# Kernel tuning notes

Hardware: AMD Instinct MI355X
Metric: run time of the kernel (lower is better)

Reference implementation:

```python
import jax, jax.numpy as jnp
import numpy as np

N = 20000       # nodes
E = 320000      # edges
D_IN = 128
H = 512
OUT = 7
EPS = 1e-5


def setup_inputs() -> dict:
    key = jax.random.key(0)
    ks = jax.random.split(key, 16)
    def lin(k, fan_in, fan_out):
        bound = 1.0 / np.sqrt(fan_in)
        kw, kb = jax.random.split(k)
        W = jax.random.uniform(kw, (fan_in, fan_out), jnp.float32, -bound, bound)
        b = jax.random.uniform(kb, (fan_out,), jnp.float32, -bound, bound)
        return W, b
    x = jax.random.normal(ks[0], (N, D_IN), jnp.float32)
    edge_index = jax.random.randint(ks[1], (2, E), 0, N, dtype=jnp.int64)
    W1, b1 = lin(ks[2], D_IN, H)
    W2, b2 = lin(ks[3], H, H)
    W3, b3 = lin(ks[4], H, H)
    W4, b4 = lin(ks[5], H, H)
    ln_gamma = jnp.ones((H,), jnp.float32)
    ln_beta = jnp.zeros((H,), jnp.float32)
    W_out, b_out = lin(ks[6], H, OUT)
    return {"x": x, "edge_index": edge_index,
            "W1": W1, "b1": b1, "W2": W2, "b2": b2,
            "W3": W3, "b3": b3, "W4": W4, "b4": b4,
            "ln_gamma": ln_gamma, "ln_beta": ln_beta,
            "W_out": W_out, "b_out": b_out}


def _gcn_layer(x, W, b, src, dst, dinv):
    # transform, then symmetric-normalized gather/scatter-add (PyG GCNConv)
    h = x @ W                                    # [N, H]
    norm = dinv[src] * dinv[dst]                 # [E+N]
    msg = h[src] * norm[:, None]                 # gather + scale
    agg = jax.ops.segment_sum(msg, dst, num_segments=N)
    return agg + b


def reference(x, edge_index, W1, b1, W2, b2, W3, b3, W4, b4,
              ln_gamma, ln_beta, W_out, b_out):
    loops = jnp.arange(N, dtype=edge_index.dtype)
    src = jnp.concatenate([edge_index[0], loops])  # A + I self loops
    dst = jnp.concatenate([edge_index[1], loops])
    deg = jax.ops.segment_sum(jnp.ones_like(src, dtype=x.dtype), dst,
                              num_segments=N)
    dinv = jnp.where(deg > 0, jax.lax.rsqrt(deg), 0.0)

    def ln(h):
        mu = h.mean(-1, keepdims=True)
        var = h.var(-1, keepdims=True)
        return (h - mu) * jax.lax.rsqrt(var + EPS) * ln_gamma + ln_beta

    for W, b in ((W1, b1), (W2, b2), (W3, b3), (W4, b4)):
        x = jax.nn.relu(ln(_gcn_layer(x, W, b, src, dst, dinv)))
    g = x.mean(axis=0)           # mean pool over nodes -> [H]
    # dropout is identity in eval mode
    return g @ W_out + b_out     # [OUT]
```

## Files before the change

kernel.cpp:

```cpp
#include <hip/hip_runtime.h>

#define HID 512
#define OUTD 7
#define EPSV 1e-5f
#define PB 256
#define PR 32

typedef __attribute__((ext_vector_type(8))) short bf16x8;
typedef __attribute__((ext_vector_type(4))) float f32x4;
typedef __attribute__((ext_vector_type(2))) float f32x2;
typedef unsigned short ushort_t;
typedef unsigned int uint_t;
typedef unsigned char uchar_t;

__device__ __forceinline__ ushort_t f2bf(float f) {
    uint_t u = __float_as_uint(f);
    u = (u + 0x7fffu + ((u >> 16) & 1u)) >> 16;
    return (ushort_t)u;
}
__device__ __forceinline__ float bflo(uint_t u) { return __uint_as_float(u << 16); }
__device__ __forceinline__ float bfhi(uint_t u) { return __uint_as_float(u & 0xffff0000u); }

__device__ __forceinline__ void acc16(const uint4& v, f32x2* a) {
    a[0] += __builtin_amdgcn_cvt_pk_f32_fp8(v.x, false);
    a[1] += __builtin_amdgcn_cvt_pk_f32_fp8(v.x, true);
    a[2] += __builtin_amdgcn_cvt_pk_f32_fp8(v.y, false);
    a[3] += __builtin_amdgcn_cvt_pk_f32_fp8(v.y, true);
    a[4] += __builtin_amdgcn_cvt_pk_f32_fp8(v.z, false);
    a[5] += __builtin_amdgcn_cvt_pk_f32_fp8(v.z, true);
    a[6] += __builtin_amdgcn_cvt_pk_f32_fp8(v.w, false);
    a[7] += __builtin_amdgcn_cvt_pk_f32_fp8(v.w, true);
}
__device__ __forceinline__ uint_t enc4(float a, float b, float c, float d) {
    uint_t r = __builtin_amdgcn_cvt_pk_fp8_f32(a, b, 0, false);
    r = __builtin_amdgcn_cvt_pk_fp8_f32(c, d, r, true);
    return r;
}

__device__ __forceinline__ void gload_lds16(const ushort_t* g, ushort_t* l) {
    __builtin_amdgcn_global_load_lds(
        (const __attribute__((address_space(1))) uint_t*)g,
        (__attribute__((address_space(3))) uint_t*)l, 16, 0, 0);
}

__global__ __launch_bounds__(256) void deg_wtrans(
        const int* __restrict__ dst, int* __restrict__ deg, int E, int degB,
        const float* __restrict__ W0, const float* __restrict__ W1,
        const float* __restrict__ W2, const float* __restrict__ W3,
        ushort_t* __restrict__ T0, ushort_t* __restrict__ T1,
        ushort_t* __restrict__ T2, ushort_t* __restrict__ T3) {
    __shared__ ushort_t tile[32][33];
    if ((int)blockIdx.x < degB) {
        int e = blockIdx.x * 256 + threadIdx.x;
        if (e < E) atomicAdd(&deg[dst[e]], 1);
        return;
    }
    int id = blockIdx.x - degB;
    const float* W; ushort_t* T; int K;
    if (id < 64)       { W = W0; T = T0; K = 128; }
    else if (id < 320) { W = W1; T = T1; K = 512; id -= 64; }
    else if (id < 576) { W = W2; T = T2; K = 512; id -= 320; }
    else               { W = W3; T = T3; K = 512; id -= 576; }
    const int tn = id & 15;
    const int tk = id >> 4;
    const int t = threadIdx.x;
    const int r = t >> 3;
    const int c4 = (t & 7) * 4;
    const float4 v = *(const float4*)&W[(size_t)(tk * 32 + r) * HID + tn * 32 + c4];
    tile[r][c4 + 0] = f2bf(v.x); tile[r][c4 + 1] = f2bf(v.y);
    tile[r][c4 + 2] = f2bf(v.z); tile[r][c4 + 3] = f2bf(v.w);
    __syncthreads();
    ushort4 ov = make_ushort4(tile[c4 + 0][r], tile[c4 + 1][r],
                              tile[c4 + 2][r], tile[c4 + 3][r]);
    *(ushort4*)&T[(size_t)(tn * 32 + r) * K + tk * 32 + c4] = ov;
}


__global__ void scan1(const int* __restrict__ deg, int* __restrict__ off,
                      int* __restrict__ partial, float* __restrict__ dinv, int N) {
    __shared__ int s[256];
    const int t = threadIdx.x;
    const int i = blockIdx.x * 256 + t;
    int d = (i < N) ? deg[i] : 0;
    if (i < N) dinv[i] = rsqrtf((float)(d + 1));
    s[t] = d;
    __syncthreads();
#pragma unroll
    for (int ofs = 1; ofs < 256; ofs <<= 1) {
        int v = (t >= ofs) ? s[t - ofs] : 0;
        __syncthreads();
        s[t] += v;
        __syncthreads();
    }
    if (i < N) off[i] = s[t] - d;
    if (t == 255) partial[blockIdx.x] = s[255];
}

__global__ void scan23(int* __restrict__ off, const int* __restrict__ partial,
                       int* __restrict__ cursor, int N, int E, int nb) {
    __shared__ int s[256];
    __shared__ int ex[256];
    const int t = threadIdx.x;
    int d = (t < nb) ? partial[t] : 0;
    s[t] = d;
    __syncthreads();
#pragma unroll
    for (int ofs = 1; ofs < 256; ofs <<= 1) {
        int v = (t >= ofs) ? s[t - ofs] : 0;
        __syncthreads();
        s[t] += v;
        __syncthreads();
    }
    ex[t] = s[t] - d;
    __syncthreads();
    int i = blockIdx.x * 256 + t;
    if (i < N) {
        int v = off[i] + ex[i >> 8];
        off[i] = v;
        cursor[i] = v;
    } else if (i == N) {
        off[N] = E;
    }
}


__global__ void fill_cvt(const int* __restrict__ src, const int* __restrict__ dst,
                         int* __restrict__ cursor, int* __restrict__ srcs, int E,
                         const float* __restrict__ x, const float* __restrict__ dinv,
                         ushort_t* __restrict__ xb, int pairs) {
    int i = blockIdx.x * blockDim.x + threadIdx.x;
    if (i < E) { int p = atomicAdd(&cursor[dst[i]], 1); srcs[p] = src[i]; return; }
    i -= E;
    if (i < pairs) {
        float dr = dinv[i >> 6];
        float a = x[2 * i] * dr, b = x[2 * i + 1] * dr;
        uint_t d = __builtin_amdgcn_cvt_pk_fp8_f32(a, b, 0, false);
        xb[i] = (ushort_t)(d & 0xffffu);
    }
}


__global__ __launch_bounds__(256) void csr_agg_512(
        const uchar_t* __restrict__ xs, const int* __restrict__ off,
        const int* __restrict__ srcs, const float* __restrict__ dinv,
        ushort_t* __restrict__ ax, int N) {
    int gtid = blockIdx.x * 256 + threadIdx.x;
    int r = gtid >> 6, lane = gtid & 63;
    if (r >= N) return;
    const int half = lane >> 5, l32 = lane & 31;
    const uint4* xb = (const uint4*)xs;
    f32x2 a[8];
#pragma unroll
    for (int q = 0; q < 8; q++) a[q] = (f32x2){0.f, 0.f};
    if (half == 0) {
        uint4 v = xb[(size_t)r * 32 + l32];
        acc16(v, a);
    }
    int e = off[r];
    const int e1 = off[r + 1];
    for (; e + 8 <= e1; e += 8) {
        int si[4]; uint4 vi[4];
#pragma unroll
        for (int j = 0; j < 4; j++) si[j] = srcs[e + 2 * j + half];
#pragma unroll
        for (int j = 0; j < 4; j++) vi[j] = xb[(size_t)si[j] * 32 + l32];
#pragma unroll
        for (int j = 0; j < 4; j++) acc16(vi[j], a);
    }
    for (; e < e1; e += 2) {
        int idx = e + half;
        bool valid = idx < e1;
        int s = srcs[valid ? idx : e];
        uint4 v = xb[(size_t)s * 32 + l32];
        if (!valid) { v.x = 0; v.y = 0; v.z = 0; v.w = 0; }
        acc16(v, a);
    }
#pragma unroll
    for (int q = 0; q < 8; q++) {
        a[q][0] += __shfl_xor(a[q][0], 32);
        a[q][1] += __shfl_xor(a[q][1], 32);
    }
    {
        float dr = dinv[r];
        const int b = half * 4;
        uint_t w0 = (uint_t)f2bf(a[b + 0][0] * dr) | ((uint_t)f2bf(a[b + 0][1] * dr) << 16);
        uint_t w1 = (uint_t)f2bf(a[b + 1][0] * dr) | ((uint_t)f2bf(a[b + 1][1] * dr) << 16);
        uint_t w2 = (uint_t)f2bf(a[b + 2][0] * dr) | ((uint_t)f2bf(a[b + 2][1] * dr) << 16);
        uint_t w3 = (uint_t)f2bf(a[b + 3][0] * dr) | ((uint_t)f2bf(a[b + 3][1] * dr) << 16);
        ((uint4*)ax)[(size_t)r * 64 + l32 * 2 + half] = make_uint4(w0, w1, w2, w3);
    }
}

__global__ __launch_bounds__(256) void csr_agg_128(
        const uchar_t* __restrict__ xs, const int* __restrict__ off,
        const int* __restrict__ srcs, const float* __restrict__ dinv,
        ushort_t* __restrict__ ax, int N) {
    int gtid = blockIdx.x * 256 + threadIdx.x;
    int r = gtid >> 6, lane = gtid & 63;
    if (r >= N) return;
    const int sub = lane >> 3, l8 = lane & 7;
    const uint4* xb = (const uint4*)xs;
    f32x2 a[8];
#pragma unroll
    for (int q = 0; q < 8; q++) a[q] = (f32x2){0.f, 0.f};
    if (sub == 0) {
        uint4 v = xb[(size_t)r * 8 + l8];
        acc16(v, a);
    }
    const int e1 = off[r + 1];
    for (int e = off[r]; e < e1; e += 8) {
        int idx = e + sub;
        bool valid = idx < e1;
        int s = srcs[valid ? idx : e];
        uint4 v = xb[(size_t)s * 8 + l8];
        if (!valid) { v.x = 0; v.y = 0; v.z = 0; v.w = 0; }
        acc16(v, a);
    }
#pragma unroll
    for (int q = 0; q < 8; q++) {
        a[q][0] += __shfl_xor(a[q][0], 8);  a[q][1] += __shfl_xor(a[q][1], 8);
        a[q][0] += __shfl_xor(a[q][0], 16); a[q][1] += __shfl_xor(a[q][1], 16);
        a[q][0] += __shfl_xor(a[q][0], 32); a[q][1] += __shfl_xor(a[q][1], 32);
    }
    if (sub < 2) {
        float dr = dinv[r];
        const int b = sub * 4;
        uint_t w0 = (uint_t)f2bf(a[b + 0][0] * dr) | ((uint_t)f2bf(a[b + 0][1] * dr) << 16);
        uint_t w1 = (uint_t)f2bf(a[b + 1][0] * dr) | ((uint_t)f2bf(a[b + 1][1] * dr) << 16);
        uint_t w2 = (uint_t)f2bf(a[b + 2][0] * dr) | ((uint_t)f2bf(a[b + 2][1] * dr) << 16);
        uint_t w3 = (uint_t)f2bf(a[b + 3][0] * dr) | ((uint_t)f2bf(a[b + 3][1] * dr) << 16);
        ((uint4*)ax)[(size_t)r * 16 + l8 * 2 + sub] = make_uint4(w0, w1, w2, w3);
    }
}


__global__ __launch_bounds__(256) void gemm_mfma(
        const ushort_t* __restrict__ A, const ushort_t* __restrict__ Wt,
        const float* __restrict__ bias, ushort_t* __restrict__ C, int M, int K, int MB) {
    __shared__ __align__(16) ushort_t AsL[128 * 64];
    __shared__ __align__(16) ushort_t BsL[128 * 64];
    const int id = blockIdx.x;
    const int mb = (id >> 5) * 8 + (id & 7);
    const int nbk = (id >> 3) & 3;
    if (mb >= MB) return;
    const int t = threadIdx.x;
    const int wave = t >> 6, lane = t & 63;
    const int m0 = mb * 128, n0 = nbk * 128;
    const int wm = (wave & 1) * 64, wn = (wave >> 1) * 64;
    const int quad = lane >> 4, l16 = lane & 15;
    const int srow = lane >> 3;
    const int schunk = (lane & 7) ^ srow;
    const int sw = (l16 & 7) << 4;

    f32x4 acc[4][4];
#pragma unroll
    for (int i = 0; i < 4; i++)
#pragma unroll
        for (int j = 0; j < 4; j++) acc[i][j] = (f32x4){0.f, 0.f, 0.f, 0.f};

    for (int k0 = 0; k0 < K; k0 += 64) {
#pragma unroll
        for (int j = 0; j < 4; j++) {
            const int c = wave * 4 + j;
            int gm = m0 + 8 * c + srow;
            if (gm >= M) gm = M - 1;
            gload_lds16(A + (size_t)gm * K + k0 + (schunk << 3), AsL + c * 512);
            gload_lds16(Wt + (size_t)(n0 + 8 * c + srow) * K + k0 + (schunk << 3),
                        BsL + c * 512);
        }
        __syncthreads();
#pragma unroll
        for (int kk = 0; kk < 2; kk++) {
            const int kb = (kk * 4 + quad) << 4;
            bf16x8 af[4], bfr[4];
#pragma unroll
            for (int jn = 0; jn < 4; jn++)
                bfr[jn] = *(const bf16x8*)((const char*)BsL
                              + (wn + jn * 16 + l16) * 128 + (kb ^ sw));
#pragma unroll
            for (int i = 0; i < 4; i++)
                af[i] = *(const bf16x8*)((const char*)AsL
                              + (wm + i * 16 + l16) * 128 + (kb ^ sw));
#pragma unroll
            for (int i = 0; i < 4; i++)
#pragma unroll
                for (int jn = 0; jn < 4; jn++)
                    acc[i][jn] = __builtin_amdgcn_mfma_f32_16x16x32_bf16(
                                     af[i], bfr[jn], acc[i][jn], 0, 0, 0);
        }
        __syncthreads();
    }
#pragma unroll
    for (int i = 0; i < 4; i++) {
#pragma unroll
        for (int jn = 0; jn < 4; jn++) {
            int gn = n0 + wn + jn * 16 + l16;
            float bv = bias[gn];
#pragma unroll
            for (int rg = 0; rg < 4; rg++) {
                int gm = m0 + wm + i * 16 + quad * 4 + rg;
                if (gm < M) C[(size_t)gm * HID + gn] = f2bf(acc[i][jn][rg] + bv);
            }
        }
    }
}


__global__ void ln_relu(const ushort_t* __restrict__ h, const float* __restrict__ gamma,
                        const float* __restrict__ beta, const float* __restrict__ dinv,
                        void* __restrict__ optr, int N) {
    int gtid = blockIdx.x * blockDim.x + threadIdx.x;
    int r = gtid >> 6, lane = gtid & 63;
    if (r >= N) return;
    uint4 v = ((const uint4*)(h + (size_t)r * HID))[lane];
    float f[8] = {bflo(v.x), bfhi(v.x), bflo(v.y), bfhi(v.y),
                  bflo(v.z), bfhi(v.z), bflo(v.w), bfhi(v.w)};
    float s = 0.f, q = 0.f;
#pragma unroll
    for (int j = 0; j < 8; j++) { s += f[j]; q += f[j] * f[j]; }
#pragma unroll
    for (int ofs = 32; ofs > 0; ofs >>= 1) {
        s += __shfl_xor(s, ofs);
        q += __shfl_xor(q, ofs);
    }
    float mu  = s * (1.0f / HID);
    float var = q * (1.0f / HID) - mu * mu;
    float rs  = rsqrtf(var + EPSV);
    float dr  = dinv[r];
    const float4* gp = (const float4*)gamma;
    const float4* bp = (const float4*)beta;
    float4 g0 = gp[2 * lane], g1 = gp[2 * lane + 1];
    float4 b0 = bp[2 * lane], b1 = bp[2 * lane + 1];
    float gg[8] = {g0.x, g0.y, g0.z, g0.w, g1.x, g1.y, g1.z, g1.w};
    float bb[8] = {b0.x, b0.y, b0.z, b0.w, b1.x, b1.y, b1.z, b1.w};
    float o[8];
#pragma unroll
    for (int j = 0; j < 8; j++)
        o[j] = fmaxf((f[j] - mu) * rs * gg[j] + bb[j], 0.f) * dr;
    uint2 ov;
    ov.x = enc4(o[0], o[1], o[2], o[3]);
    ov.y = enc4(o[4], o[5], o[6], o[7]);
    ((uint2*)optr)[(size_t)r * 64 + lane] = ov;
}


__global__ __launch_bounds__(256) void ln_pool(
        const ushort_t* __restrict__ h, const float* __restrict__ gamma,
        const float* __restrict__ beta, float* __restrict__ pbuf, int N) {
    __shared__ float sred[4][64][8];
    const int t = threadIdx.x;
    const int sub = t >> 6, lane = t & 63;
    const float4* gp = (const float4*)gamma;
    const float4* bp = (const float4*)beta;
    float4 g0 = gp[2 * lane], g1 = gp[2 * lane + 1];
    float4 b0 = bp[2 * lane], b1 = bp[2 * lane + 1];
    float gg[8] = {g0.x, g0.y, g0.z, g0.w, g1.x, g1.y, g1.z, g1.w};
    float bb[8] = {b0.x, b0.y, b0.z, b0.w, b1.x, b1.y, b1.z, b1.w};
    float colacc[8] = {0.f, 0.f, 0.f, 0.f, 0.f, 0.f, 0.f, 0.f};
    const int step = PB * 4;
    for (int r = blockIdx.x * 4 + sub; r < N; r += step) {
        uint4 v = ((const uint4*)(h + (size_t)r * HID))[lane];
        float f[8] = {bflo(v.x), bfhi(v.x), bflo(v.y), bfhi(v.y),
                      bflo(v.z), bfhi(v.z), bflo(v.w), bfhi(v.w)};
        float s = 0.f, q = 0.f;
#pragma unroll
        for (int j = 0; j < 8; j++) { s += f[j]; q += f[j] * f[j]; }
#pragma unroll
        for (int ofs = 32; ofs > 0; ofs >>= 1) {
            s += __shfl_xor(s, ofs);
            q += __shfl_xor(q, ofs);
        }
        float mu  = s * (1.0f / HID);
        float var = q * (1.0f / HID) - mu * mu;
        float rs  = rsqrtf(var + EPSV);
#pragma unroll
        for (int j = 0; j < 8; j++)
            colacc[j] += fmaxf((f[j] - mu) * rs * gg[j] + bb[j], 0.f);
    }
#pragma unroll
    for (int j = 0; j < 8; j++) sred[sub][lane][j] = colacc[j];
    __syncthreads();
    if (sub == 0) {
        float4 o0, o1;
        o0.x = sred[0][lane][0] + sred[1][lane][0] + sred[2][lane][0] + sred[3][lane][0];
        o0.y = sred[0][lane][1] + sred[1][lane][1] + sred[2][lane][1] + sred[3][lane][1];
        o0.z = sred[0][lane][2] + sred[1][lane][2] + sred[2][lane][2] + sred[3][lane][2];
        o0.w = sred[0][lane][3] + sred[1][lane][3] + sred[2][lane][3] + sred[3][lane][3];
        o1.x = sred[0][lane][4] + sred[1][lane][4] + sred[2][lane][4] + sred[3][lane][4];
        o1.y = sred[0][lane][5] + sred[1][lane][5] + sred[2][lane][5] + sred[3][lane][5];
        o1.z = sred[0][lane][6] + sred[1][lane][6] + sred[2][lane][6] + sred[3][lane][6];
        o1.w = sred[0][lane][7] + sred[1][lane][7] + sred[2][lane][7] + sred[3][lane][7];
        float* pb = pbuf + (size_t)blockIdx.x * HID + lane * 8;
        ((float4*)pb)[0] = o0;
        ((float4*)pb)[1] = o1;
    }
}


__global__ __launch_bounds__(256) void pool_reduce(
        const float* __restrict__ pbuf, float* __restrict__ pbuf2) {
    const int t = threadIdx.x;
    const int b = blockIdx.x;
    const int R = PB / PR;
    float2 s = make_float2(0.f, 0.f);
#pragma unroll
    for (int u = 0; u < R; u++) {
        const float2 v = ((const float2*)(pbuf + (size_t)(b * R + u) * HID))[t];
        s.x += v.x; s.y += v.y;
    }
    ((float2*)(pbuf2 + (size_t)b * HID))[t] = s;
}


__global__ void out_kernel(const float* __restrict__ pbuf2, const float* __restrict__ Wout,
                           const float* __restrict__ bout, float* __restrict__ out, int N) {
    __shared__ float red[256];
    int t = threadIdx.x;
    float g0 = 0.f, g1 = 0.f;
#pragma unroll
    for (int p = 0; p < PR; p += 8) {
#pragma unroll
        for (int u = 0; u < 8; u++) {
            const float2 v = ((const float2*)(pbuf2 + (size_t)(p + u) * HID))[t];
            g0 += v.x; g1 += v.y;
        }
    }
    float invn = 1.0f / (float)N;
    for (int o = 0; o < OUTD; o++) {
        float pr = g0 * Wout[(2 * t) * OUTD + o] + g1 * Wout[(2 * t + 1) * OUTD + o];
        red[t] = pr;
        __syncthreads();
        for (int sft = 128; sft > 0; sft >>= 1) {
            if (t < sft) red[t] += red[t + sft];
            __syncthreads();
        }
        if (t == 0) out[o] = red[0] * invn + bout[o];
        __syncthreads();
    }
}


extern "C" void kernel_launch(void* const* d_in, const int* in_sizes, int n_in,
                              void* d_out, int out_size, void* d_ws, size_t ws_size,
                              hipStream_t stream) {
    const float* x  = (const float*)d_in[0];
    const int*   ei = (const int*)d_in[1];
    const int N = in_sizes[0] / 128;
    const int E = in_sizes[1] / 2;
    const int* src = ei;
    const int* dst = ei + E;
    const float* Ws[4] = {(const float*)d_in[2], (const float*)d_in[4],
                          (const float*)d_in[6], (const float*)d_in[8]};
    const float* bs[4] = {(const float*)d_in[3], (const float*)d_in[5],
                          (const float*)d_in[7], (const float*)d_in[9]};
    const float* gamma = (const float*)d_in[10];
    const float* beta  = (const float*)d_in[11];
    const float* Wout  = (const float*)d_in[12];
    const float* bout  = (const float*)d_in[13];
    float* out = (float*)d_out;

    char* p = (char*)d_ws;
    ushort_t* axb = (ushort_t*)p;  p += sizeof(ushort_t) * (size_t)N * HID;
    ushort_t* hb  = (ushort_t*)p;  p += sizeof(ushort_t) * (size_t)N * HID;
    uchar_t*  ho8 = (uchar_t*)p;   p += (size_t)N * HID;
    uchar_t*  xb8 = ho8;
    ushort_t* Wt[4];
    Wt[0] = (ushort_t*)p;          p += sizeof(ushort_t) * 128 * HID;
    Wt[1] = (ushort_t*)p;          p += sizeof(ushort_t) * HID * HID;
    Wt[2] = (ushort_t*)p;          p += sizeof(ushort_t) * HID * HID;
    Wt[3] = (ushort_t*)p;          p += sizeof(ushort_t) * HID * HID;
    float* dinv  = (float*)p;      p += sizeof(float) * N;
    float* pbuf  = (float*)p;      p += sizeof(float) * PB * HID;
    float* pbuf2 = (float*)p;      p += sizeof(float) * PR * HID;
    int* deg    = (int*)p;         p += sizeof(int) * N;
    int* off    = (int*)p;         p += sizeof(int) * (N + 4);
    int* cursor = (int*)p;         p += sizeof(int) * N;
    int* partial= (int*)p;         p += sizeof(int) * 256;
    int* srcs   = (int*)p;

    const int nb = (N + 255) / 256;
    const int MB = (N + 127) / 128;
    const int gemm_blocks = 32 * ((MB + 7) / 8);
    const int degB = (E + 255) / 256;

    hipMemsetAsync(deg, 0, sizeof(int) * N, stream);
    deg_wtrans<<<degB + 832, 256, 0, stream>>>(dst, deg, E, degB,
                                               Ws[0], Ws[1], Ws[2], Ws[3],
                                               Wt[0], Wt[1], Wt[2], Wt[3]);
    scan1<<<nb, 256, 0, stream>>>(deg, off, partial, dinv, N);
    scan23<<<(N + 256) / 256, 256, 0, stream>>>(off, partial, cursor, N, E, nb);
    {
        int pairs = N * 64;
        int tot = E + pairs;
        fill_cvt<<<(tot + 255) / 256, 256, 0, stream>>>(src, dst, cursor, srcs, E,
                                                        x, dinv, (ushort_t*)xb8, pairs);
    }

    for (int l = 0; l < 4; l++) {
        const int K = (l == 0) ? 128 : HID;
        if (l == 0)
            csr_agg_128<<<(N * 64 + 255) / 256, 256, 0, stream>>>(xb8, off, srcs, dinv, axb, N);
        else
            csr_agg_512<<<(N * 64 + 255) / 256, 256, 0, stream>>>(ho8, off, srcs, dinv, axb, N);
        gemm_mfma<<<gemm_blocks, 256, 0, stream>>>(axb, Wt[l], bs[l], hb, N, K, MB);
        if (l < 3)
            ln_relu<<<(N * 64 + 255) / 256, 256, 0, stream>>>(hb, gamma, beta, dinv, ho8, N);
        else
            ln_pool<<<PB, 256, 0, stream>>>(hb, gamma, beta, pbuf, N);
    }
    pool_reduce<<<PR, 256, 0, stream>>>(pbuf, pbuf2);
    out_kernel<<<1, 256, 0, stream>>>(pbuf2, Wout, bout, out, N);
}
```

Baseline: 362.5 us.

## Bucket CSR neighbor lists by source range and fold pool reduction into output kernel

Edge counts are now kept per (destination, source-chunk) pair across 10 chunks, and the fill step places each edge into its chunk's slot. Each node's neighbor list therefore comes out roughly sorted by source index, which should improve cache locality for the feature gathers in the aggregation kernels. Separately, the pool_reduce kernel is removed and out_kernel sums all 256 partial rows itself, saving one launch but running that sum in a single block. In exchange, the degree and fill passes do twice the atomics and need ten times the count and cursor memory.

```diff
diff --git a/kernel.cpp b/kernel.cpp
--- a/kernel.cpp
+++ b/kernel.cpp
@@ -4,7 +4,7 @@
 #define OUTD 7
 #define EPSV 1e-5f
 #define PB 256
-#define PR 32
+#define NCH 10
 
 typedef __attribute__((ext_vector_type(8))) short bf16x8;
 typedef __attribute__((ext_vector_type(4))) float f32x4;
@@ -44,7 +44,8 @@
 }
 
 __global__ __launch_bounds__(256) void deg_wtrans(
-        const int* __restrict__ dst, int* __restrict__ deg, int E, int degB,
+        const int* __restrict__ src, const int* __restrict__ dst,
+        int* __restrict__ deg, int* __restrict__ deg10, int E, int degB, int sh,
         const float* __restrict__ W0, const float* __restrict__ W1,
         const float* __restrict__ W2, const float* __restrict__ W3,
         ushort_t* __restrict__ T0, ushort_t* __restrict__ T1,
@@ -52,7 +53,11 @@
     __shared__ ushort_t tile[32][33];
     if ((int)blockIdx.x < degB) {
         int e = blockIdx.x * 256 + threadIdx.x;
-        if (e < E) atomicAdd(&deg[dst[e]], 1);
+        if (e < E) {
+            int d = dst[e];
+            atomicAdd(&deg[d], 1);
+            atomicAdd(&deg10[d * NCH + (src[e] >> sh)], 1);
+        }
         return;
     }
     int id = blockIdx.x - degB;
@@ -97,7 +102,8 @@
 }
 
 __global__ void scan23(int* __restrict__ off, const int* __restrict__ partial,
-                       int* __restrict__ cursor, int N, int E, int nb) {
+                       const int* __restrict__ deg10, int* __restrict__ cursor10,
+                       int N, int E, int nb) {
     __shared__ int s[256];
     __shared__ int ex[256];
     const int t = threadIdx.x;
@@ -117,7 +123,12 @@
     if (i < N) {
         int v = off[i] + ex[i >> 8];
         off[i] = v;
-        cursor[i] = v;
+        int base = v;
+#pragma unroll
+        for (int c = 0; c < NCH; c++) {
+            cursor10[i * NCH + c] = base;
+            base += deg10[i * NCH + c];
+        }
     } else if (i == N) {
         off[N] = E;
     }
@@ -125,11 +136,16 @@
 
 
 __global__ void fill_cvt(const int* __restrict__ src, const int* __restrict__ dst,
-                         int* __restrict__ cursor, int* __restrict__ srcs, int E,
+                         int* __restrict__ cursor10, int* __restrict__ srcs, int E, int sh,
                          const float* __restrict__ x, const float* __restrict__ dinv,
                          ushort_t* __restrict__ xb, int pairs) {
     int i = blockIdx.x * blockDim.x + threadIdx.x;
-    if (i < E) { int p = atomicAdd(&cursor[dst[i]], 1); srcs[p] = src[i]; return; }
+    if (i < E) {
+        int sv = src[i];
+        int p = atomicAdd(&cursor10[dst[i] * NCH + (sv >> sh)], 1);
+        srcs[p] = sv;
+        return;
+    }
     i -= E;
     if (i < pairs) {
         float dr = dinv[i >> 6];
@@ -397,33 +413,15 @@
 }
 
 
-__global__ __launch_bounds__(256) void pool_reduce(
-        const float* __restrict__ pbuf, float* __restrict__ pbuf2) {
-    const int t = threadIdx.x;
-    const int b = blockIdx.x;
-    const int R = PB / PR;
-    float2 s = make_float2(0.f, 0.f);
-#pragma unroll
-    for (int u = 0; u < R; u++) {
-        const float2 v = ((const float2*)(pbuf + (size_t)(b * R + u) * HID))[t];
-        s.x += v.x; s.y += v.y;
-    }
-    ((float2*)(pbuf2 + (size_t)b * HID))[t] = s;
-}
-
-
-__global__ void out_kernel(const float* __restrict__ pbuf2, const float* __restrict__ Wout,
+__global__ void out_kernel(const float* __restrict__ pbuf, const float* __restrict__ Wout,
                            const float* __restrict__ bout, float* __restrict__ out, int N) {
     __shared__ float red[256];
     int t = threadIdx.x;
     float g0 = 0.f, g1 = 0.f;
-#pragma unroll
-    for (int p = 0; p < PR; p += 8) {
-#pragma unroll
-        for (int u = 0; u < 8; u++) {
-            const float2 v = ((const float2*)(pbuf2 + (size_t)(p + u) * HID))[t];
-            g0 += v.x; g1 += v.y;
-        }
+#pragma unroll 8
+    for (int p = 0; p < PB; p++) {
+        const float2 v = ((const float2*)(pbuf + (size_t)p * HID))[t];
+        g0 += v.x; g1 += v.y;
     }
     float invn = 1.0f / (float)N;
     for (int o = 0; o < OUTD; o++) {
@@ -459,6 +457,9 @@
     const float* bout  = (const float*)d_in[13];
     float* out = (float*)d_out;
 
+    int sh = 11;
+    while (((N - 1) >> sh) >= NCH) sh++;
+
     char* p = (char*)d_ws;
     ushort_t* axb = (ushort_t*)p;  p += sizeof(ushort_t) * (size_t)N * HID;
     ushort_t* hb  = (ushort_t*)p;  p += sizeof(ushort_t) * (size_t)N * HID;
@@ -471,28 +472,28 @@
     Wt[3] = (ushort_t*)p;          p += sizeof(ushort_t) * HID * HID;
     float* dinv  = (float*)p;      p += sizeof(float) * N;
     float* pbuf  = (float*)p;      p += sizeof(float) * PB * HID;
-    float* pbuf2 = (float*)p;      p += sizeof(float) * PR * HID;
-    int* deg    = (int*)p;         p += sizeof(int) * N;
-    int* off    = (int*)p;         p += sizeof(int) * (N + 4);
-    int* cursor = (int*)p;         p += sizeof(int) * N;
-    int* partial= (int*)p;         p += sizeof(int) * 256;
-    int* srcs   = (int*)p;
+    int* deg     = (int*)p;        p += sizeof(int) * N;
+    int* deg10   = (int*)p;        p += sizeof(int) * N * NCH;
+    int* cursor10= (int*)p;        p += sizeof(int) * N * NCH;
+    int* off     = (int*)p;        p += sizeof(int) * (N + 4);
+    int* partial = (int*)p;        p += sizeof(int) * 256;
+    int* srcs    = (int*)p;
 
     const int nb = (N + 255) / 256;
     const int MB = (N + 127) / 128;
     const int gemm_blocks = 32 * ((MB + 7) / 8);
     const int degB = (E + 255) / 256;
 
-    hipMemsetAsync(deg, 0, sizeof(int) * N, stream);
-    deg_wtrans<<<degB + 832, 256, 0, stream>>>(dst, deg, E, degB,
+    hipMemsetAsync(deg, 0, sizeof(int) * N * (1 + NCH), stream);
+    deg_wtrans<<<degB + 832, 256, 0, stream>>>(src, dst, deg, deg10, E, degB, sh,
                                                Ws[0], Ws[1], Ws[2], Ws[3],
                                                Wt[0], Wt[1], Wt[2], Wt[3]);
     scan1<<<nb, 256, 0, stream>>>(deg, off, partial, dinv, N);
-    scan23<<<(N + 256) / 256, 256, 0, stream>>>(off, partial, cursor, N, E, nb);
+    scan23<<<(N + 256) / 256, 256, 0, stream>>>(off, partial, deg10, cursor10, N, E, nb);
     {
         int pairs = N * 64;
         int tot = E + pairs;
-        fill_cvt<<<(tot + 255) / 256, 256, 0, stream>>>(src, dst, cursor, srcs, E,
+        fill_cvt<<<(tot + 255) / 256, 256, 0, stream>>>(src, dst, cursor10, srcs, E, sh,
                                                         x, dinv, (ushort_t*)xb8, pairs);
     }
 
@@ -508,6 +509,5 @@
         else
             ln_pool<<<PB, 256, 0, stream>>>(hb, gamma, beta, pbuf, N);
     }
-    pool_reduce<<<PR, 256, 0, stream>>>(pbuf, pbuf2);
-    out_kernel<<<1, 256, 0, stream>>>(pbuf2, Wout, bout, out, N);
-}
+    out_kernel<<<1, 256, 0, stream>>>(pbuf, Wout, bout, out, N);
+}
```

Result: slower. 380.7 us (+5.0%).

## Fuse LayerNorm+ReLU and pooling into GEMM via last-block-per-row-tile epilogue

Applied to the files above, without the earlier changes.

Each of the four column-tile GEMM blocks for a 128-row tile increments an atomic counter after writing its part. The last block to arrive re-reads the full 128x512 bf16 rows and applies LayerNorm+ReLU: it writes the fp8 scaled output, or in the final layer accumulates per-tile column sums for pooling. This removes the separate ln_relu, ln_pool and pool_reduce launches. The cost is that the LN work is serialized onto one block per row tile, and it adds atomics and threadfences. The out_kernel now sums the roughly 157 per-tile partial buffers serially.

```diff
diff --git a/kernel.cpp b/kernel.cpp
--- a/kernel.cpp
+++ b/kernel.cpp
@@ -3,8 +3,7 @@
 #define HID 512
 #define OUTD 7
 #define EPSV 1e-5f
-#define PB 256
-#define PR 32
+#define MBPAD 256
 
 typedef __attribute__((ext_vector_type(8))) short bf16x8;
 typedef __attribute__((ext_vector_type(4))) float f32x4;
@@ -234,11 +233,17 @@
 }
 
 
+template<int POOL>
 __global__ __launch_bounds__(256) void gemm_mfma(
         const ushort_t* __restrict__ A, const ushort_t* __restrict__ Wt,
-        const float* __restrict__ bias, ushort_t* __restrict__ C, int M, int K, int MB) {
+        const float* __restrict__ bias, const float* __restrict__ gamma,
+        const float* __restrict__ beta, const float* __restrict__ dinv,
+        ushort_t* __restrict__ C, uchar_t* __restrict__ out8,
+        float* __restrict__ pbuf, uint_t* __restrict__ tcnt,
+        int M, int K, int MB) {
     __shared__ __align__(16) ushort_t AsL[128 * 64];
     __shared__ __align__(16) ushort_t BsL[128 * 64];
+    __shared__ uint_t lastf;
     const int id = blockIdx.x;
     const int mb = (id >> 5) * 8 + (id & 7);
     const int nbk = (id >> 3) & 3;
@@ -303,63 +308,28 @@
             }
         }
     }
-}
-
-
-__global__ void ln_relu(const ushort_t* __restrict__ h, const float* __restrict__ gamma,
-                        const float* __restrict__ beta, const float* __restrict__ dinv,
-                        void* __restrict__ optr, int N) {
-    int gtid = blockIdx.x * blockDim.x + threadIdx.x;
-    int r = gtid >> 6, lane = gtid & 63;
-    if (r >= N) return;
-    uint4 v = ((const uint4*)(h + (size_t)r * HID))[lane];
-    float f[8] = {bflo(v.x), bfhi(v.x), bflo(v.y), bfhi(v.y),
-                  bflo(v.z), bfhi(v.z), bflo(v.w), bfhi(v.w)};
-    float s = 0.f, q = 0.f;
-#pragma unroll
-    for (int j = 0; j < 8; j++) { s += f[j]; q += f[j] * f[j]; }
-#pragma unroll
-    for (int ofs = 32; ofs > 0; ofs >>= 1) {
-        s += __shfl_xor(s, ofs);
-        q += __shfl_xor(q, ofs);
-    }
-    float mu  = s * (1.0f / HID);
-    float var = q * (1.0f / HID) - mu * mu;
-    float rs  = rsqrtf(var + EPSV);
-    float dr  = dinv[r];
+
+    __syncthreads();
+    if (t == 0) {
+        __threadfence();
+        lastf = (atomicAdd(&tcnt[mb], 1u) == 3u) ? 1u : 0u;
+    }
+    __syncthreads();
+    if (!lastf) return;
+    __threadfence();
+
     const float4* gp = (const float4*)gamma;
     const float4* bp = (const float4*)beta;
-    float4 g0 = gp[2 * lane], g1 = gp[2 * lane + 1];
-    float4 b0 = bp[2 * lane], b1 = bp[2 * lane + 1];
-    float gg[8] = {g0.x, g0.y, g0.z, g0.w, g1.x, g1.y, g1.z, g1.w};
-    float bb[8] = {b0.x, b0.y, b0.z, b0.w, b1.x, b1.y, b1.z, b1.w};
-    float o[8];
-#pragma unroll
-    for (int j = 0; j < 8; j++)
-        o[j] = fmaxf((f[j] - mu) * rs * gg[j] + bb[j], 0.f) * dr;
-    uint2 ov;
-    ov.x = enc4(o[0], o[1], o[2], o[3]);
-    ov.y = enc4(o[4], o[5], o[6], o[7]);
-    ((uint2*)optr)[(size_t)r * 64 + lane] = ov;
-}
-
-
-__global__ __launch_bounds__(256) void ln_pool(
-        const ushort_t* __restrict__ h, const float* __restrict__ gamma,
-        const float* __restrict__ beta, float* __restrict__ pbuf, int N) {
-    __shared__ float sred[4][64][8];
-    const int t = threadIdx.x;
-    const int sub = t >> 6, lane = t & 63;
-    const float4* gp = (const float4*)gamma;
-    const float4* bp = (const float4*)beta;
-    float4 g0 = gp[2 * lane], g1 = gp[2 * lane + 1];
-    float4 b0 = bp[2 * lane], b1 = bp[2 * lane + 1];
-    float gg[8] = {g0.x, g0.y, g0.z, g0.w, g1.x, g1.y, g1.z, g1.w};
-    float bb[8] = {b0.x, b0.y, b0.z, b0.w, b1.x, b1.y, b1.z, b1.w};
+    float4 g4a = gp[2 * lane], g4b = gp[2 * lane + 1];
+    float4 b4a = bp[2 * lane], b4b = bp[2 * lane + 1];
+    float gg[8] = {g4a.x, g4a.y, g4a.z, g4a.w, g4b.x, g4b.y, g4b.z, g4b.w};
+    float bb[8] = {b4a.x, b4a.y, b4a.z, b4a.w, b4b.x, b4b.y, b4b.z, b4b.w};
     float colacc[8] = {0.f, 0.f, 0.f, 0.f, 0.f, 0.f, 0.f, 0.f};
-    const int step = PB * 4;
-    for (int r = blockIdx.x * 4 + sub; r < N; r += step) {
-        uint4 v = ((const uint4*)(h + (size_t)r * HID))[lane];
+
+    for (int rr = wave; rr < 128; rr += 4) {
+        const int gm = m0 + rr;
+        if (gm >= M) continue;
+        uint4 v = ((const uint4*)(C + (size_t)gm * HID))[lane];
         float f[8] = {bflo(v.x), bfhi(v.x), bflo(v.y), bfhi(v.y),
                       bflo(v.z), bfhi(v.z), bflo(v.w), bfhi(v.w)};
         float s = 0.f, q = 0.f;
@@ -373,57 +343,51 @@
         float mu  = s * (1.0f / HID);
         float var = q * (1.0f / HID) - mu * mu;
         float rs  = rsqrtf(var + EPSV);
-#pragma unroll
-        for (int j = 0; j < 8; j++)
-            colacc[j] += fmaxf((f[j] - mu) * rs * gg[j] + bb[j], 0.f);
-    }
-#pragma unroll
-    for (int j = 0; j < 8; j++) sred[sub][lane][j] = colacc[j];
-    __syncthreads();
-    if (sub == 0) {
-        float4 o0, o1;
-        o0.x = sred[0][lane][0] + sred[1][lane][0] + sred[2][lane][0] + sred[3][lane][0];
-        o0.y = sred[0][lane][1] + sred[1][lane][1] + sred[2][lane][1] + sred[3][lane][1];
-        o0.z = sred[0][lane][2] + sred[1][lane][2] + sred[2][lane][2] + sred[3][lane][2];
-        o0.w = sred[0][lane][3] + sred[1][lane][3] + sred[2][lane][3] + sred[3][lane][3];
-        o1.x = sred[0][lane][4] + sred[1][lane][4] + sred[2][lane][4] + sred[3][lane][4];
-        o1.y = sred[0][lane][5] + sred[1][lane][5] + sred[2][lane][5] + sred[3][lane][5];
-        o1.z = sred[0][lane][6] + sred[1][lane][6] + sred[2][lane][6] + sred[3][lane][6];
-        o1.w = sred[0][lane][7] + sred[1][lane][7] + sred[2][lane][7] + sred[3][lane][7];
-        float* pb = pbuf + (size_t)blockIdx.x * HID + lane * 8;
-        ((float4*)pb)[0] = o0;
-        ((float4*)pb)[1] = o1;
-    }
-}
-
-
-__global__ __launch_bounds__(256) void pool_reduce(
-        const float* __restrict__ pbuf, float* __restrict__ pbuf2) {
-    const int t = threadIdx.x;
-    const int b = blockIdx.x;
-    const int R = PB / PR;
-    float2 s = make_float2(0.f, 0.f);
-#pragma unroll
-    for (int u = 0; u < R; u++) {
-        const float2 v = ((const float2*)(pbuf + (size_t)(b * R + u) * HID))[t];
-        s.x += v.x; s.y += v.y;
-    }
-    ((float2*)(pbuf2 + (size_t)b * HID))[t] = s;
-}
-
-
-__global__ void out_kernel(const float* __restrict__ pbuf2, const float* __restrict__ Wout,
-                           const float* __restrict__ bout, float* __restrict__ out, int N) {
+        if (POOL) {
+#pragma unroll
+            for (int j = 0; j < 8; j++)
+                colacc[j] += fmaxf((f[j] - mu) * rs * gg[j] + bb[j], 0.f);
+        } else {
+            float dr = dinv[gm];
+            float o[8];
+#pragma unroll
+            for (int j = 0; j < 8; j++)
+                o[j] = fmaxf((f[j] - mu) * rs * gg[j] + bb[j], 0.f) * dr;
+            uint2 ov;
+            ov.x = enc4(o[0], o[1], o[2], o[3]);
+            ov.y = enc4(o[4], o[5], o[6], o[7]);
+            ((uint2*)out8)[(size_t)gm * 64 + lane] = ov;
+        }
+    }
+
+    if (POOL) {
+        float (*sred)[64][8] = (float(*)[64][8])AsL;
+#pragma unroll
+        for (int j = 0; j < 8; j++) sred[wave][lane][j] = colacc[j];
+        __syncthreads();
+        if (wave == 0) {
+            float o[8];
+#pragma unroll
+            for (int j = 0; j < 8; j++)
+                o[j] = sred[0][lane][j] + sred[1][lane][j]
+                     + sred[2][lane][j] + sred[3][lane][j];
+            float* pb = pbuf + (size_t)mb * HID + lane * 8;
+            ((float4*)pb)[0] = make_float4(o[0], o[1], o[2], o[3]);
+            ((float4*)pb)[1] = make_float4(o[4], o[5], o[6], o[7]);
+        }
+    }
+}
+
+
+__global__ void out_kernel(const float* __restrict__ pbuf, const float* __restrict__ Wout,
+                           const float* __restrict__ bout, float* __restrict__ out,
+                           int N, int MB) {
     __shared__ float red[256];
     int t = threadIdx.x;
     float g0 = 0.f, g1 = 0.f;
-#pragma unroll
-    for (int p = 0; p < PR; p += 8) {
-#pragma unroll
-        for (int u = 0; u < 8; u++) {
-            const float2 v = ((const float2*)(pbuf2 + (size_t)(p + u) * HID))[t];
-            g0 += v.x; g1 += v.y;
-        }
+    for (int p = 0; p < MB; p++) {
+        const float2 v = ((const float2*)(pbuf + (size_t)p * HID))[t];
+        g0 += v.x; g1 += v.y;
     }
     float invn = 1.0f / (float)N;
     for (int o = 0; o < OUTD; o++) {
@@ -459,6 +423,8 @@
     const float* bout  = (const float*)d_in[13];
     float* out = (float*)d_out;
 
+    const int MB = (N + 127) / 128;
+
     char* p = (char*)d_ws;
     ushort_t* axb = (ushort_t*)p;  p += sizeof(ushort_t) * (size_t)N * HID;
     ushort_t* hb  = (ushort_t*)p;  p += sizeof(ushort_t) * (size_t)N * HID;
@@ -470,20 +436,19 @@
     Wt[2] = (ushort_t*)p;          p += sizeof(ushort_t) * HID * HID;
     Wt[3] = (ushort_t*)p;          p += sizeof(ushort_t) * HID * HID;
     float* dinv  = (float*)p;      p += sizeof(float) * N;
-    float* pbuf  = (float*)p;      p += sizeof(float) * PB * HID;
-    float* pbuf2 = (float*)p;      p += sizeof(float) * PR * HID;
-    int* deg    = (int*)p;         p += sizeof(int) * N;
-    int* off    = (int*)p;         p += sizeof(int) * (N + 4);
-    int* cursor = (int*)p;         p += sizeof(int) * N;
-    int* partial= (int*)p;         p += sizeof(int) * 256;
-    int* srcs   = (int*)p;
+    float* pbuf  = (float*)p;      p += sizeof(float) * (size_t)(MB + 4) * HID;
+    int* deg     = (int*)p;        p += sizeof(int) * N;
+    uint_t* tcnt = (uint_t*)p;     p += sizeof(uint_t) * 4 * MBPAD;
+    int* off     = (int*)p;        p += sizeof(int) * (N + 4);
+    int* cursor  = (int*)p;        p += sizeof(int) * N;
+    int* partial = (int*)p;        p += sizeof(int) * 256;
+    int* srcs    = (int*)p;
 
     const int nb = (N + 255) / 256;
-    const int MB = (N + 127) / 128;
     const int gemm_blocks = 32 * ((MB + 7) / 8);
     const int degB = (E + 255) / 256;
 
-    hipMemsetAsync(deg, 0, sizeof(int) * N, stream);
+    hipMemsetAsync(deg, 0, sizeof(int) * N + sizeof(uint_t) * 4 * MBPAD, stream);
     deg_wtrans<<<degB + 832, 256, 0, stream>>>(dst, deg, E, degB,
                                                Ws[0], Ws[1], Ws[2], Ws[3],
                                                Wt[0], Wt[1], Wt[2], Wt[3]);
@@ -502,12 +467,14 @@
             csr_agg_128<<<(N * 64 + 255) / 256, 256, 0, stream>>>(xb8, off, srcs, dinv, axb, N);
         else
             csr_agg_512<<<(N * 64 + 255) / 256, 256, 0, stream>>>(ho8, off, srcs, dinv, axb, N);
-        gemm_mfma<<<gemm_blocks, 256, 0, stream>>>(axb, Wt[l], bs[l], hb, N, K, MB);
         if (l < 3)
-            ln_relu<<<(N * 64 + 255) / 256, 256, 0, stream>>>(hb, gamma, beta, dinv, ho8, N);
+            gemm_mfma<0><<<gemm_blocks, 256, 0, stream>>>(
+                axb, Wt[l], bs[l], gamma, beta, dinv, hb, ho8, pbuf,
+                tcnt + l * MBPAD, N, K, MB);
         else
-            ln_pool<<<PB, 256, 0, stream>>>(hb, gamma, beta, pbuf, N);
-    }
-    pool_reduce<<<PR, 256, 0, stream>>>(pbuf, pbuf2);
-    out_kernel<<<1, 256, 0, stream>>>(pbuf2, Wout, bout, out, N);
-}
+            gemm_mfma<1><<<gemm_blocks, 256, 0, stream>>>(
+                axb, Wt[l], bs[l], gamma, beta, dinv, hb, ho8, pbuf,
+                tcnt + l * MBPAD, N, K, MB);
+    }
+    out_kernel<<<1, 256, 0, stream>>>(pbuf, Wout, bout, out, N, MB);
+}
```

Result: slower. 652.3 us (+80.0%).
